# Kernel tuning notes

Hardware: AMD Instinct MI355X
Metric: run time of the kernel (lower is better)

## Reference

```python
import jax, jax.numpy as jnp
import numpy as np

N = 8192        # nodes
NFEAT = 256     # input feature dim
NHID = 64       # per-head hidden dim
NHEADS = 4
NCLASS = 121    # PPI label count
ALPHA = 0.2     # LeakyReLU negative slope
NEG_INF = jnp.float32(-9e15)  # pyGAT's mask fill value


def setup_inputs() -> dict:
    key = jax.random.key(0)
    k = jax.random.split(key, 6)
    x = jax.random.normal(k[0], (N, NFEAT), dtype=jnp.float32)
    adj = (jax.random.uniform(k[1], (N, N)) < 0.01).astype(jnp.float32)
    idx = jnp.arange(N)
    adj = adj.at[idx, idx].set(1.0)
    # per-head first-layer params: W [H, nfeat, nhid], a [H, 2*nhid]
    Ws = jax.random.normal(k[2], (NHEADS, NFEAT, NHID), dtype=jnp.float32) * 0.1
    a_heads = jax.random.normal(k[3], (NHEADS, 2 * NHID), dtype=jnp.float32) * 0.1
    # output attention layer params
    W_out = jax.random.normal(k[4], (NHEADS * NHID, NCLASS), dtype=jnp.float32) * 0.1
    a_out = jax.random.normal(k[5], (2 * NCLASS,), dtype=jnp.float32) * 0.1
    return {"x": x, "adj": adj, "Ws": Ws, "a_heads": a_heads,
            "W_out": W_out, "a_out": a_out}


def _gat_head(x, adj, W, a, concat):
    # Dense GraphAttentionLayer (pyGAT), eval mode (dropout off).
    Wh = x @ W                                   # [N, d]
    d = W.shape[1]
    f_src = Wh @ a[:d]                           # [N]  score contribution of node i
    f_dst = Wh @ a[d:]                           # [N]  score contribution of node j
    e = jax.nn.leaky_relu(f_src[:, None] + f_dst[None, :], ALPHA)  # [N, N]
    e = jnp.where(adj > 0, e, NEG_INF)
    att = jax.nn.softmax(e, axis=-1)             # [N, N]
    h = att @ Wh                                 # [N, d]
    return jax.nn.elu(h) if concat else h


def reference(x, adj, Ws, a_heads, W_out, a_out):
    # first multi-head layer (concat=True, elu), vmapped over heads
    heads = jax.vmap(lambda W, a: _gat_head(x, adj, W, a, True))(Ws, a_heads)  # [H, N, nhid]
    h_cat = jnp.transpose(heads, (1, 0, 2)).reshape(x.shape[0], NHEADS * NHID)  # torch.cat(dim=1)
    # output attention layer (concat=False -> raw aggregation)
    return _gat_head(h_cat, adj, W_out, a_out, False)  # [N, nclass]
```

## Files before the change

kernel.cpp:

```cpp
#include <hip/hip_runtime.h>
#include <math.h>

#define N_NODES 8192
#define NFEAT 256
#define NHID 64
#define NHEADS 4
#define NCLASS 121
#define NCPAD 128
#define CAP 256
#define LRALPHA 0.2f

#define GEMM_BLOCKS 128
#define CSR_BASE    GEMM_BLOCKS
#define PAD_BLOCK   (CSR_BASE + N_NODES)

__global__ __launch_bounds__(256) void fused_A(const float* __restrict__ adj,
                                               const float* __restrict__ x,
                                               const float* __restrict__ Ws,
                                               const float* __restrict__ a_heads,
                                               const float* __restrict__ Wout,
                                               const float* __restrict__ aout,
                                               int* __restrict__ nbr,
                                               int* __restrict__ deg,
                                               float* __restrict__ Wh1,
                                               float* __restrict__ fs1,
                                               float* __restrict__ fd1,
                                               float* __restrict__ Wpad,
                                               float* __restrict__ apad) {
    __shared__ __align__(16) char smem[64 * 132 * 4];
    int b = blockIdx.x;
    int tid = threadIdx.x;

    if (b >= CSR_BASE && b < PAD_BLOCK) {
        int row = b - CSR_BASE;
        int* cnt = (int*)smem;
        if (tid == 0) *cnt = 0;
        __syncthreads();
        const float4* arow = (const float4*)(adj + (size_t)row * N_NODES);
        for (int j4 = tid; j4 < N_NODES / 4; j4 += 256) {
            float4 v = arow[j4];
            if (v.x > 0.f) { int s = atomicAdd(cnt, 1); if (s < CAP) nbr[row * CAP + s] = j4 * 4 + 0; }
            if (v.y > 0.f) { int s = atomicAdd(cnt, 1); if (s < CAP) nbr[row * CAP + s] = j4 * 4 + 1; }
            if (v.z > 0.f) { int s = atomicAdd(cnt, 1); if (s < CAP) nbr[row * CAP + s] = j4 * 4 + 2; }
            if (v.w > 0.f) { int s = atomicAdd(cnt, 1); if (s < CAP) nbr[row * CAP + s] = j4 * 4 + 3; }
        }
        __syncthreads();
        if (tid == 0) deg[row] = *cnt < CAP ? *cnt : CAP;
        return;
    }
    if (b == PAD_BLOCK) {
        for (int idx = tid; idx < 256 * NCPAD; idx += 256) {
            int k = idx >> 7, c = idx & 127;
            Wpad[idx] = (c < NCLASS) ? Wout[k * NCLASS + c] : 0.f;
        }
        if (tid < 256) {
            int c = tid & 127;
            float v = 0.f;
            if (c < NCLASS) v = (tid < 128) ? aout[c] : aout[NCLASS + c];
            apad[tid] = v;
        }
        return;
    }

    float (*xs)[132] = (float(*)[132])smem;
    int r0 = b * 64;
    int d = tid & 63;
    int rb = (tid >> 6) * 16;
    float acc[NHEADS][16];
#pragma unroll
    for (int h = 0; h < NHEADS; h++)
#pragma unroll
        for (int r = 0; r < 16; r++) acc[h][r] = 0.f;

    const float* Wd = Ws + d;
    for (int ph = 0; ph < 2; ph++) {
        for (int t = tid; t < 64 * 32; t += 256) {
            int r = t >> 5, c4 = t & 31;
            *(float4*)&xs[r][c4 * 4] =
                *(const float4*)(x + (size_t)(r0 + r) * NFEAT + ph * 128 + c4 * 4);
        }
        __syncthreads();
        for (int k4 = 0; k4 < 128; k4 += 4) {
            int kg = ph * 128 + k4;
            float bb[NHEADS][4];
#pragma unroll
            for (int h = 0; h < NHEADS; h++)
#pragma unroll
                for (int kk = 0; kk < 4; kk++)
                    bb[h][kk] = Wd[(size_t)h * NFEAT * NHID + (kg + kk) * NHID];
#pragma unroll
            for (int r = 0; r < 16; r++) {
                float4 a = *(const float4*)&xs[rb + r][k4];
#pragma unroll
                for (int h = 0; h < NHEADS; h++)
                    acc[h][r] += a.x * bb[h][0] + a.y * bb[h][1] +
                                 a.z * bb[h][2] + a.w * bb[h][3];
            }
        }
        __syncthreads();
    }
#pragma unroll
    for (int h = 0; h < NHEADS; h++)
#pragma unroll
        for (int r = 0; r < 16; r++)
            Wh1[(size_t)(r0 + rb + r) * 256 + h * NHID + d] = acc[h][r];
    float asrc[NHEADS], adst[NHEADS];
#pragma unroll
    for (int h = 0; h < NHEADS; h++) {
        asrc[h] = a_heads[h * 2 * NHID + d];
        adst[h] = a_heads[h * 2 * NHID + NHID + d];
    }
#pragma unroll
    for (int h = 0; h < NHEADS; h++) {
#pragma unroll
        for (int r = 0; r < 16; r++) {
            float s = acc[h][r] * asrc[h];
            float dd = acc[h][r] * adst[h];
#pragma unroll
            for (int o = 32; o > 0; o >>= 1) { s += __shfl_xor(s, o); dd += __shfl_xor(dd, o); }
            if (d == 0) {
                fs1[h * N_NODES + r0 + rb + r] = s;
                fd1[h * N_NODES + r0 + rb + r] = dd;
            }
        }
    }
}

__global__ __launch_bounds__(256) void attn_agg1(const int* __restrict__ nbr,
                                                 const int* __restrict__ deg,
                                                 const float* __restrict__ Wh1,
                                                 const float* __restrict__ fs1,
                                                 const float* __restrict__ fd1,
                                                 float* __restrict__ hcat) {
    int i = blockIdx.x;
    int h = threadIdx.x >> 6, lane = threadIdx.x & 63;
    __shared__ float ebuf[NHEADS][CAP + 1];
    __shared__ int nbrs[CAP];
    __shared__ float inv_s[NHEADS];
    __shared__ float part[NHEADS][256];
    int dg = deg[i];
    for (int t = threadIdx.x; t < dg; t += 256) nbrs[t] = nbr[i * CAP + t];
    __syncthreads();
    float fsi = fs1[h * N_NODES + i];
    const float* fdh = fd1 + h * N_NODES;
    float m = -3.4e38f;
    for (int t = lane; t < dg; t += 64) {
        float e = fsi + fdh[nbrs[t]];
        e = e > 0.f ? e : LRALPHA * e;
        ebuf[h][t] = e;
        m = fmaxf(m, e);
    }
#pragma unroll
    for (int o = 32; o > 0; o >>= 1) m = fmaxf(m, __shfl_xor(m, o));
    float s = 0.f;
    for (int t = lane; t < dg; t += 64) {
        float p = __expf(ebuf[h][t] - m);
        ebuf[h][t] = p;
        s += p;
    }
#pragma unroll
    for (int o = 32; o > 0; o >>= 1) s += __shfl_xor(s, o);
    if (lane == 0) inv_s[h] = 1.f / s;
    __syncthreads();
    int w = h;
    int hh = lane >> 4;
    float4 acc = make_float4(0.f, 0.f, 0.f, 0.f);
    int t = w;
    for (; t + 8 <= dg; t += 8) {
        int j0 = nbrs[t], j1 = nbrs[t + 4];
        float4 v0 = ((const float4*)(Wh1 + (size_t)j0 * 256))[lane];
        float4 v1 = ((const float4*)(Wh1 + (size_t)j1 * 256))[lane];
        float p0 = ebuf[hh][t], p1 = ebuf[hh][t + 4];
        acc.x += p0 * v0.x; acc.y += p0 * v0.y; acc.z += p0 * v0.z; acc.w += p0 * v0.w;
        acc.x += p1 * v1.x; acc.y += p1 * v1.y; acc.z += p1 * v1.z; acc.w += p1 * v1.w;
    }
    for (; t < dg; t += 4) {
        int j = nbrs[t];
        float4 v = ((const float4*)(Wh1 + (size_t)j * 256))[lane];
        float p = ebuf[hh][t];
        acc.x += p * v.x; acc.y += p * v.y; acc.z += p * v.z; acc.w += p * v.w;
    }
    ((float4*)part[w])[lane] = acc;
    __syncthreads();
    int dim = threadIdx.x;
    float r = part[0][dim] + part[1][dim] + part[2][dim] + part[3][dim];
    r *= inv_s[dim >> 6];
    r = r > 0.f ? r : expm1f(r);
    hcat[(size_t)i * 256 + dim] = r;
}

__global__ __launch_bounds__(256) void gemm2(const float* __restrict__ hcat,
                                             const float* __restrict__ Wpad,
                                             const float* __restrict__ apad,
                                             float* __restrict__ Wh2,
                                             float* __restrict__ fs2,
                                             float* __restrict__ fd2) {
    int r0 = blockIdx.x * 64;
    __shared__ float xs[64][260];
    for (int t = threadIdx.x; t < 64 * 64; t += 256) {
        int r = t >> 6, c4 = t & 63;
        *(float4*)&xs[r][c4 * 4] = *(const float4*)(hcat + (size_t)(r0 + r) * 256 + c4 * 4);
    }
    __syncthreads();
    int lane = threadIdx.x & 63;
    int c0 = lane * 2;
    int rb = (threadIdx.x >> 6) * 16;
    float acc0[16] = {}, acc1[16] = {};
    for (int k4 = 0; k4 < 256; k4 += 4) {
        float2 b0 = *(const float2*)&Wpad[(k4 + 0) * NCPAD + c0];
        float2 b1 = *(const float2*)&Wpad[(k4 + 1) * NCPAD + c0];
        float2 b2 = *(const float2*)&Wpad[(k4 + 2) * NCPAD + c0];
        float2 b3 = *(const float2*)&Wpad[(k4 + 3) * NCPAD + c0];
#pragma unroll
        for (int r = 0; r < 16; r++) {
            float4 a = *(const float4*)&xs[rb + r][k4];
            acc0[r] += a.x * b0.x + a.y * b1.x + a.z * b2.x + a.w * b3.x;
            acc1[r] += a.x * b0.y + a.y * b1.y + a.z * b2.y + a.w * b3.y;
        }
    }
#pragma unroll
    for (int r = 0; r < 16; r++)
        *(float2*)&Wh2[(size_t)(r0 + rb + r) * NCPAD + c0] = make_float2(acc0[r], acc1[r]);
    float as0 = apad[c0], as1 = apad[c0 + 1];
    float ad0 = apad[128 + c0], ad1 = apad[128 + c0 + 1];
#pragma unroll
    for (int r = 0; r < 16; r++) {
        float s = acc0[r] * as0 + acc1[r] * as1;
        float dd = acc0[r] * ad0 + acc1[r] * ad1;
#pragma unroll
        for (int o = 32; o > 0; o >>= 1) { s += __shfl_xor(s, o); dd += __shfl_xor(dd, o); }
        if (lane == 0) { fs2[r0 + rb + r] = s; fd2[r0 + rb + r] = dd; }
    }
}

__global__ __launch_bounds__(256) void attn_agg2(const int* __restrict__ nbr,
                                                 const int* __restrict__ deg,
                                                 const float* __restrict__ Wh2,
                                                 const float* __restrict__ fs2,
                                                 const float* __restrict__ fd2,
                                                 float* __restrict__ out) {
    int i = blockIdx.x;
    int w = threadIdx.x >> 6, lane = threadIdx.x & 63;
    __shared__ float ebuf[CAP];
    __shared__ int nbrs[CAP];
    __shared__ float red[4];
    __shared__ float part[4][128];
    __shared__ float inv_s;
    int dg = deg[i];
    for (int t = threadIdx.x; t < dg; t += 256) nbrs[t] = nbr[i * CAP + t];
    __syncthreads();
    float fsi = fs2[i];
    float m = -3.4e38f;
    for (int t = threadIdx.x; t < dg; t += 256) {
        float e = fsi + fd2[nbrs[t]];
        e = e > 0.f ? e : LRALPHA * e;
        ebuf[t] = e;
        m = fmaxf(m, e);
    }
#pragma unroll
    for (int o = 32; o > 0; o >>= 1) m = fmaxf(m, __shfl_xor(m, o));
    if (lane == 0) red[w] = m;
    __syncthreads();
    m = fmaxf(fmaxf(red[0], red[1]), fmaxf(red[2], red[3]));
    float s = 0.f;
    for (int t = threadIdx.x; t < dg; t += 256) {
        float p = __expf(ebuf[t] - m);
        ebuf[t] = p;
        s += p;
    }
#pragma unroll
    for (int o = 32; o > 0; o >>= 1) s += __shfl_xor(s, o);
    __syncthreads();
    if (lane == 0) red[w] = s;
    __syncthreads();
    if (threadIdx.x == 0) inv_s = 1.f / (red[0] + red[1] + red[2] + red[3]);
    __syncthreads();
    float2 acc = make_float2(0.f, 0.f);
    int t = w;
    for (; t + 8 <= dg; t += 8) {
        int j0 = nbrs[t], j1 = nbrs[t + 4];
        float2 v0 = ((const float2*)(Wh2 + (size_t)j0 * NCPAD))[lane];
        float2 v1 = ((const float2*)(Wh2 + (size_t)j1 * NCPAD))[lane];
        float p0 = ebuf[t], p1 = ebuf[t + 4];
        acc.x += p0 * v0.x; acc.y += p0 * v0.y;
        acc.x += p1 * v1.x; acc.y += p1 * v1.y;
    }
    for (; t < dg; t += 4) {
        int j = nbrs[t];
        float2 v = ((const float2*)(Wh2 + (size_t)j * NCPAD))[lane];
        float p = ebuf[t];
        acc.x += p * v.x; acc.y += p * v.y;
    }
    ((float2*)part[w])[lane] = acc;
    __syncthreads();
    if (threadIdx.x < NCPAD) {
        int dim = threadIdx.x;
        float r = (part[0][dim] + part[1][dim] + part[2][dim] + part[3][dim]) * inv_s;
        if (dim < NCLASS) out[(size_t)i * NCLASS + dim] = r;
    }
}


extern "C" void kernel_launch(void* const* d_in, const int* in_sizes, int n_in,
                              void* d_out, int out_size, void* d_ws, size_t ws_size,
                              hipStream_t stream) {
    const float* x       = (const float*)d_in[0];
    const float* adj     = (const float*)d_in[1];
    const float* Ws      = (const float*)d_in[2];
    const float* a_heads = (const float*)d_in[3];
    const float* Wout    = (const float*)d_in[4];
    const float* aout    = (const float*)d_in[5];
    float* out = (float*)d_out;

    char* ws = (char*)d_ws;
    size_t off = 0;
    auto alloc = [&](size_t bytes) { void* p = ws + off; off = (off + bytes + 255) & ~(size_t)255; return p; };
    int*   nbr  = (int*)  alloc((size_t)N_NODES * CAP * 4);
    int*   deg  = (int*)  alloc((size_t)N_NODES * 4);
    float* Wh1  = (float*)alloc((size_t)N_NODES * NHEADS * NHID * 4);
    float* fs1  = (float*)alloc((size_t)NHEADS * N_NODES * 4);
    float* fd1  = (float*)alloc((size_t)NHEADS * N_NODES * 4);
    float* hcat = (float*)alloc((size_t)N_NODES * NHEADS * NHID * 4);
    float* Wh2  = (float*)alloc((size_t)N_NODES * NCPAD * 4);
    float* fs2  = (float*)alloc((size_t)N_NODES * 4);
    float* fd2  = (float*)alloc((size_t)N_NODES * 4);
    float* Wpad = (float*)alloc((size_t)256 * NCPAD * 4);
    float* apad = (float*)alloc((size_t)256 * 4);

    fused_A<<<PAD_BLOCK + 1, 256, 0, stream>>>(adj, x, Ws, a_heads, Wout, aout,
                                               nbr, deg, Wh1, fs1, fd1, Wpad, apad);
    attn_agg1<<<N_NODES, 256, 0, stream>>>(nbr, deg, Wh1, fs1, fd1, hcat);
    gemm2<<<N_NODES / 64, 256, 0, stream>>>(hcat, Wpad, apad, Wh2, fs2, fd2);
    attn_agg2<<<N_NODES, 256, 0, stream>>>(nbr, deg, Wh2, fs2, fd2, out);
}
```

Before: 593.5 us.

## Split CSR build into ballot-compacted kernel and unroll aggregation gathers deeper

Splits the fused kernel into a dedicated CSR builder and a separate GEMM/padding kernel. The CSR builder loads all eight float4s of each adjacency row up front and compacts neighbours with wavefront ballot plus popcount, so each wave issues one shared atomic per column batch instead of one atomic per nonzero. Both aggregation kernels now gather four neighbour rows per iteration instead of two, to put more loads in flight. The extra launch adds a little overhead, and the ballot loop runs 32 steps per thread even when rows are sparse.

```diff
diff --git a/kernel.cpp b/kernel.cpp
--- a/kernel.cpp
+++ b/kernel.cpp
@@ -10,45 +10,54 @@
 #define CAP 256
 #define LRALPHA 0.2f
 
-#define GEMM_BLOCKS 128
-#define CSR_BASE    GEMM_BLOCKS
-#define PAD_BLOCK   (CSR_BASE + N_NODES)
-
-__global__ __launch_bounds__(256) void fused_A(const float* __restrict__ adj,
-                                               const float* __restrict__ x,
-                                               const float* __restrict__ Ws,
-                                               const float* __restrict__ a_heads,
-                                               const float* __restrict__ Wout,
-                                               const float* __restrict__ aout,
-                                               int* __restrict__ nbr,
-                                               int* __restrict__ deg,
-                                               float* __restrict__ Wh1,
-                                               float* __restrict__ fs1,
-                                               float* __restrict__ fd1,
-                                               float* __restrict__ Wpad,
-                                               float* __restrict__ apad) {
-    __shared__ __align__(16) char smem[64 * 132 * 4];
+__global__ __launch_bounds__(256) void build_csr(const float* __restrict__ adj,
+                                                 int* __restrict__ nbr,
+                                                 int* __restrict__ deg) {
+    int row = blockIdx.x;
+    int tid = threadIdx.x;
+    int lane = tid & 63;
+    __shared__ int cnt;
+    if (tid == 0) cnt = 0;
+    __syncthreads();
+    const float4* arow = (const float4*)(adj + (size_t)row * N_NODES);
+    float4 v[8];
+#pragma unroll
+    for (int it = 0; it < 8; it++) v[it] = arow[tid + it * 256];
+#pragma unroll
+    for (int it = 0; it < 8; it++) {
+        int jb = (tid + it * 256) * 4;
+#pragma unroll
+        for (int c = 0; c < 4; c++) {
+            float val = (c == 0) ? v[it].x : (c == 1) ? v[it].y : (c == 2) ? v[it].z : v[it].w;
+            bool p = val > 0.f;
+            unsigned long long mk = __ballot(p);
+            int nset = __popcll(mk);
+            int wbase = 0;
+            if (lane == 0 && nset) wbase = atomicAdd(&cnt, nset);
+            wbase = __shfl(wbase, 0);
+            if (p) {
+                int pos = wbase + __popcll(mk & ((1ull << lane) - 1ull));
+                if (pos < CAP) nbr[row * CAP + pos] = jb + c;
+            }
+        }
+    }
+    __syncthreads();
+    if (tid == 0) deg[row] = cnt < CAP ? cnt : CAP;
+}
+
+__global__ __launch_bounds__(256) void gemm1(const float* __restrict__ x,
+                                             const float* __restrict__ Ws,
+                                             const float* __restrict__ a_heads,
+                                             const float* __restrict__ Wout,
+                                             const float* __restrict__ aout,
+                                             float* __restrict__ Wh1,
+                                             float* __restrict__ fs1,
+                                             float* __restrict__ fd1,
+                                             float* __restrict__ Wpad,
+                                             float* __restrict__ apad) {
     int b = blockIdx.x;
     int tid = threadIdx.x;
-
-    if (b >= CSR_BASE && b < PAD_BLOCK) {
-        int row = b - CSR_BASE;
-        int* cnt = (int*)smem;
-        if (tid == 0) *cnt = 0;
-        __syncthreads();
-        const float4* arow = (const float4*)(adj + (size_t)row * N_NODES);
-        for (int j4 = tid; j4 < N_NODES / 4; j4 += 256) {
-            float4 v = arow[j4];
-            if (v.x > 0.f) { int s = atomicAdd(cnt, 1); if (s < CAP) nbr[row * CAP + s] = j4 * 4 + 0; }
-            if (v.y > 0.f) { int s = atomicAdd(cnt, 1); if (s < CAP) nbr[row * CAP + s] = j4 * 4 + 1; }
-            if (v.z > 0.f) { int s = atomicAdd(cnt, 1); if (s < CAP) nbr[row * CAP + s] = j4 * 4 + 2; }
-            if (v.w > 0.f) { int s = atomicAdd(cnt, 1); if (s < CAP) nbr[row * CAP + s] = j4 * 4 + 3; }
-        }
-        __syncthreads();
-        if (tid == 0) deg[row] = *cnt < CAP ? *cnt : CAP;
-        return;
-    }
-    if (b == PAD_BLOCK) {
+    if (b == N_NODES / 64) {
         for (int idx = tid; idx < 256 * NCPAD; idx += 256) {
             int k = idx >> 7, c = idx & 127;
             Wpad[idx] = (c < NCLASS) ? Wout[k * NCLASS + c] : 0.f;
@@ -61,8 +70,7 @@
         }
         return;
     }
-
-    float (*xs)[132] = (float(*)[132])smem;
+    __shared__ float xs[64][132];
     int r0 = b * 64;
     int d = tid & 63;
     int rb = (tid >> 6) * 16;
@@ -166,13 +174,18 @@
     int hh = lane >> 4;
     float4 acc = make_float4(0.f, 0.f, 0.f, 0.f);
     int t = w;
-    for (; t + 8 <= dg; t += 8) {
-        int j0 = nbrs[t], j1 = nbrs[t + 4];
+    for (; t + 16 <= dg; t += 16) {
+        int j0 = nbrs[t], j1 = nbrs[t + 4], j2 = nbrs[t + 8], j3 = nbrs[t + 12];
         float4 v0 = ((const float4*)(Wh1 + (size_t)j0 * 256))[lane];
         float4 v1 = ((const float4*)(Wh1 + (size_t)j1 * 256))[lane];
+        float4 v2 = ((const float4*)(Wh1 + (size_t)j2 * 256))[lane];
+        float4 v3 = ((const float4*)(Wh1 + (size_t)j3 * 256))[lane];
         float p0 = ebuf[hh][t], p1 = ebuf[hh][t + 4];
+        float p2 = ebuf[hh][t + 8], p3 = ebuf[hh][t + 12];
         acc.x += p0 * v0.x; acc.y += p0 * v0.y; acc.z += p0 * v0.z; acc.w += p0 * v0.w;
         acc.x += p1 * v1.x; acc.y += p1 * v1.y; acc.z += p1 * v1.z; acc.w += p1 * v1.w;
+        acc.x += p2 * v2.x; acc.y += p2 * v2.y; acc.z += p2 * v2.z; acc.w += p2 * v2.w;
+        acc.x += p3 * v3.x; acc.y += p3 * v3.y; acc.z += p3 * v3.z; acc.w += p3 * v3.w;
     }
     for (; t < dg; t += 4) {
         int j = nbrs[t];
@@ -277,13 +290,17 @@
     __syncthreads();
     float2 acc = make_float2(0.f, 0.f);
     int t = w;
-    for (; t + 8 <= dg; t += 8) {
-        int j0 = nbrs[t], j1 = nbrs[t + 4];
+    for (; t + 16 <= dg; t += 16) {
+        int j0 = nbrs[t], j1 = nbrs[t + 4], j2 = nbrs[t + 8], j3 = nbrs[t + 12];
         float2 v0 = ((const float2*)(Wh2 + (size_t)j0 * NCPAD))[lane];
         float2 v1 = ((const float2*)(Wh2 + (size_t)j1 * NCPAD))[lane];
-        float p0 = ebuf[t], p1 = ebuf[t + 4];
+        float2 v2 = ((const float2*)(Wh2 + (size_t)j2 * NCPAD))[lane];
+        float2 v3 = ((const float2*)(Wh2 + (size_t)j3 * NCPAD))[lane];
+        float p0 = ebuf[t], p1 = ebuf[t + 4], p2 = ebuf[t + 8], p3 = ebuf[t + 12];
         acc.x += p0 * v0.x; acc.y += p0 * v0.y;
         acc.x += p1 * v1.x; acc.y += p1 * v1.y;
+        acc.x += p2 * v2.x; acc.y += p2 * v2.y;
+        acc.x += p3 * v3.x; acc.y += p3 * v3.y;
     }
     for (; t < dg; t += 4) {
         int j = nbrs[t];
@@ -327,8 +344,9 @@
     float* Wpad = (float*)alloc((size_t)256 * NCPAD * 4);
     float* apad = (float*)alloc((size_t)256 * 4);
 
-    fused_A<<<PAD_BLOCK + 1, 256, 0, stream>>>(adj, x, Ws, a_heads, Wout, aout,
-                                               nbr, deg, Wh1, fs1, fd1, Wpad, apad);
+    build_csr<<<N_NODES, 256, 0, stream>>>(adj, nbr, deg);
+    gemm1<<<N_NODES / 64 + 1, 256, 0, stream>>>(x, Ws, a_heads, Wout, aout,
+                                                Wh1, fs1, fd1, Wpad, apad);
     attn_agg1<<<N_NODES, 256, 0, stream>>>(nbr, deg, Wh1, fs1, fd1, hcat);
     gemm2<<<N_NODES / 64, 256, 0, stream>>>(hcat, Wpad, apad, Wh2, fs2, fd2);
     attn_agg2<<<N_NODES, 256, 0, stream>>>(nbr, deg, Wh2, fs2, fd2, out);
```

Measured after the change: 560.3 us. 1.06x faster.
